# Performance work log

Hardware: AMD Instinct MI355X
Metric: run time of the kernel (lower is better)

Reference implementation:

```python
import jax, jax.numpy as jnp
import numpy as np

B, H_IMG, W_IMG = 8, 64, 64
C, HEADS, SR, MSG = 128, 4, 4, 4
N0 = H_IMG * W_IMG


def _linear(x, w, b):
    return x @ w.T + b


def _layernorm(x, g, b, eps=1e-5):
    mu = jnp.mean(x, -1, keepdims=True)
    var = jnp.mean(jnp.square(x - mu), -1, keepdims=True)
    return (x - mu) * jax.lax.rsqrt(var + eps) * g + b


def _conv2d(x, w, b, stride, pad, groups=1):
    y = jax.lax.conv_general_dilated(
        x, w, (stride, stride), [(pad, pad), (pad, pad)],
        dimension_numbers=("NCHW", "OIHW", "NCHW"), feature_group_count=groups)
    return y + b[None, :, None, None]


def setup_inputs():
    key = jax.random.key(0)
    ks = jax.random.split(key, 16)
    def nrm(k, shape, std=0.02):
        return jax.random.normal(k, shape, jnp.float32) * std
    z = lambda *s: jnp.zeros(s, jnp.float32)
    return {
        "x": jax.random.normal(ks[0], (B, N0, C), jnp.float32),
        "msg_tokens": jax.random.normal(ks[1], (B, MSG, C), jnp.float32),
        "Wq": nrm(ks[2], (C, C)), "bq": z(C),
        "sr1_w": nrm(ks[3], (C, C, 4, 4), float(np.sqrt(2.0 / (16 * C)))), "sr1_b": z(C),
        "ln1_g": jnp.ones((C,), jnp.float32), "ln1_b": z(C),
        "sr2_w": nrm(ks[4], (C, C, 2, 2), float(np.sqrt(2.0 / (4 * C)))), "sr2_b": z(C),
        "ln2_g": jnp.ones((C,), jnp.float32), "ln2_b": z(C),
        "kv1_w": nrm(ks[5], (C, C)), "kv1_b": z(C),
        "kv2_w": nrm(ks[6], (C, C)), "kv2_b": z(C),
        "lc1_w": nrm(ks[7], (C // 2, 1, 3, 3), float(np.sqrt(2.0 / 9.0))), "lc1_b": z(C // 2),
        "lc2_w": nrm(ks[8], (C // 2, 1, 3, 3), float(np.sqrt(2.0 / 9.0))), "lc2_b": z(C // 2),
        "proj_w": nrm(ks[9], (C, C)), "proj_b": z(C),
        "H": H_IMG, "W": W_IMG,
    }


def reference(x, msg_tokens, Wq, bq, sr1_w, sr1_b, ln1_g, ln1_b,
              sr2_w, sr2_b, ln2_g, ln2_b, kv1_w, kv1_b, kv2_w, kv2_b,
              lc1_w, lc1_b, lc2_w, lc2_b, proj_w, proj_b, H, W):
    Bsz, _, Cc = x.shape
    m = msg_tokens.shape[1]
    h = HEADS
    dh = Cc // h
    scale = dh ** -0.5
    x_q = jnp.concatenate([x, msg_tokens], axis=1)       # [B, N, C]
    N = x_q.shape[1]
    q = _linear(x_q, Wq, bq).reshape(Bsz, N, h, dh).transpose(0, 2, 1, 3)  # [B,h,N,dh]
    x_img = x.transpose(0, 2, 1).reshape(Bsz, Cc, H, W)

    def branch(sr_w, sr_b, ln_g, ln_b, kv_w, kv_b, lc_w, lc_b, q_half, stride):
        Hr, Wr = H // stride, W // stride
        L = Hr * Wr
        # spatial reduction conv -> tokens
        xr = _conv2d(x_img, sr_w, sr_b, stride, 0).reshape(Bsz, Cc, L).transpose(0, 2, 1)
        # message tokens pass through the SR conv via summed weights
        msg_r = jnp.einsum('bnc,oc->bno', msg_tokens, sr_w.sum((-1, -2))) + sr_b
        xk = jax.nn.gelu(_layernorm(jnp.concatenate([xr, msg_r], 1), ln_g, ln_b), approximate=False)
        kv = _linear(xk, kv_w, kv_b).reshape(Bsz, L + m, 2, h // 2, dh).transpose(2, 0, 3, 1, 4)
        k, v = kv[0], kv[1]                               # [B, h/2, L+m, dh]
        attn = jax.nn.softmax(jnp.einsum('bhnd,bhld->bhnl', q_half, k) * scale, axis=-1)
        # fused depthwise conv on the spatial part of V (message tokens bypass)
        v_flat = v.transpose(0, 2, 1, 3).reshape(Bsz, L + m, Cc // 2).transpose(0, 2, 1)  # [B,C/2,L+m]
        lc = _conv2d(v_flat[:, :, :L].reshape(Bsz, Cc // 2, Hr, Wr), lc_w, lc_b, 1, 1,
                     groups=Cc // 2).reshape(Bsz, Cc // 2, L)
        v_add = jnp.concatenate([lc, v_flat[:, :, L:]], axis=2)
        v = v + v_add.reshape(Bsz, h // 2, dh, L + m).transpose(0, 1, 3, 2)
        return jnp.einsum('bhnl,bhld->bhnd', attn, v).transpose(0, 2, 1, 3).reshape(Bsz, N, Cc // 2)

    x1 = branch(sr1_w, sr1_b, ln1_g, ln1_b, kv1_w, kv1_b, lc1_w, lc1_b, q[:, :h // 2], SR)
    x2 = branch(sr2_w, sr2_b, ln2_g, ln2_b, kv2_w, kv2_b, lc2_w, lc2_b, q[:, h // 2:], SR // 2)
    out = _linear(jnp.concatenate([x1, x2], -1), proj_w, proj_b)
    out = x_q + out                                       # identity = x_q, drop_path = Identity
    return out[:, :-m], out[:, -m:]
```

## Files before the change

kernel.cpp:

```cpp
#include <hip/hip_runtime.h>
#include <math.h>

#define BB 8
#define CC 128
#define N0 4096
#define MSGN 4
#define NTOT 4100
#define IMG 64
#define NPAD 4112
#define QTILES 257
#define LMP1 320
#define LMP2 1088

#define OFF_WFQ    0
#define OFF_WFKV1  8192
#define OFF_WFKV2  16384
#define OFF_WFPROJ 24576
#define OFF_WFSR1  32768
#define OFF_WFSR2  163840
#define OFF_QH     196608
#define OFF_XK1    2301952
#define OFF_XK2    2435072
#define OFF_KV1O   2961408
#define OFF_KV2O   3227648
#define OFF_KH1    4280320
#define OFF_VT1    4362240
#define OFF_KH2    4444160
#define OFF_VT2    4722688
#define OFF_XP0    5001216
#define OFF_XP1    7102464
#define OFF_L0     2301952
#define OFF_L1     2433280

typedef _Float16 half8v __attribute__((ext_vector_type(8)));
typedef _Float16 half4v __attribute__((ext_vector_type(4)));
typedef float f32x4 __attribute__((ext_vector_type(4)));

__device__ __forceinline__ size_t af_idx(int m, int k, int Kc) {
    return ((size_t)((m >> 4) * Kc + (k >> 5)) * 64 + ((k >> 3) & 3) * 16 + (m & 15)) * 8 + (k & 7);
}

__global__ void prep_weights(const float* __restrict__ Wq, const float* __restrict__ kv1,
                             const float* __restrict__ kv2, const float* __restrict__ proj,
                             const float* __restrict__ sr1w, const float* __restrict__ sr2w,
                             float* __restrict__ ws, _Float16* __restrict__ Qh) {
    int u = blockIdx.x * blockDim.x + threadIdx.x;
    if (u >= 49152) {
        int idx = u - 49152;
        if (idx >= BB * 4 * (NPAD - NTOT) * 32) return;
        int d = idx & 31;
        int rest = idx >> 5;
        int n = NTOT + rest % (NPAD - NTOT);
        int rest2 = rest / (NPAD - NTOT);
        int hg = rest2 & 3;
        int b = rest2 >> 2;
        Qh[((size_t)(b * 4 + hg) * NPAD + n) * 32 + d] = (_Float16)0.f;
        return;
    }
    int seg, base;
    const float* w = nullptr;
    _Float16* dst;
    if (u < 2048)        { seg = 0; base = u;          w = Wq;   dst = (_Float16*)(ws + OFF_WFQ); }
    else if (u < 4096)   { seg = 0; base = u - 2048;   w = kv1;  dst = (_Float16*)(ws + OFF_WFKV1); }
    else if (u < 6144)   { seg = 0; base = u - 4096;   w = kv2;  dst = (_Float16*)(ws + OFF_WFKV2); }
    else if (u < 8192)   { seg = 0; base = u - 6144;   w = proj; dst = (_Float16*)(ws + OFF_WFPROJ); }
    else if (u < 40960)  { seg = 1; base = u - 8192;   w = sr1w; dst = (_Float16*)(ws + OFF_WFSR1); }
    else                 { seg = 2; base = u - 40960;  w = sr2w; dst = (_Float16*)(ws + OFF_WFSR2); }
    int lane = base & 63;
    int t = (base >> 6) & 7;
    int kc = base >> 9;
    int n = t * 16 + (lane & 15);
    int k0 = kc * 32 + (lane >> 4) * 8;
    half8v val;
    #pragma unroll
    for (int j = 0; j < 8; ++j) {
        int k = k0 + j;
        float v;
        if (seg == 0) v = w[n * 128 + k];
        else if (seg == 1) v = w[(n * 128 + (k & 127)) * 16 + (k >> 7)];
        else v = w[(n * 128 + (k & 127)) * 4 + (k >> 7)];
        val[j] = (_Float16)v;
    }
    *(half8v*)(dst + (size_t)base * 8) = val;
}

template<int S, int WR, int LL, int LM, int KW>
__device__ __forceinline__ void sr_partial(
    int mtile, int kcbase, int lane, const float* __restrict__ x,
    const float* __restrict__ msg, const _Float16* __restrict__ Wf, f32x4 acc[8]) {
    int m15 = lane & 15, quadk = lane >> 4;
    int m = mtile * 16 + m15;
    bool valid = m < BB * LM;
    const float* base = x;
    bool isimg = false;
    if (valid) {
        int b = m / LM, tok = m - b * LM;
        if (tok < LL) {
            int hr = tok / WR, wr = tok - hr * WR;
            base = x + ((size_t)b * N0 + hr * S * IMG + wr * S) * 128;
            isimg = true;
        } else {
            base = msg + ((size_t)b * MSGN + (tok - LL)) * 128;
        }
    }
    const half8v* Bp = (const half8v*)Wf + lane;
    for (int kk = 0; kk < KW; ++kk) {
        int kc = kcbase + kk;
        int k0 = (kc * 4 + quadk) * 8;
        int c = k0 & 127, ij = k0 >> 7;
        half8v a;
        if (valid) {
            int off;
            if (isimg) {
                int ki = ij / S, kj = ij - ki * S;
                off = (ki * IMG + kj) * 128 + c;
            } else off = c;
            const float4* p4 = (const float4*)(base + off);
            float4 f0 = p4[0], f1 = p4[1];
            a[0] = (_Float16)f0.x; a[1] = (_Float16)f0.y; a[2] = (_Float16)f0.z; a[3] = (_Float16)f0.w;
            a[4] = (_Float16)f1.x; a[5] = (_Float16)f1.y; a[6] = (_Float16)f1.z; a[7] = (_Float16)f1.w;
        } else {
            #pragma unroll
            for (int j = 0; j < 8; ++j) a[j] = (_Float16)0.f;
        }
        #pragma unroll
        for (int t = 0; t < 8; ++t)
            acc[t] = __builtin_amdgcn_mfma_f32_16x16x32_f16(a, Bp[(size_t)(kc * 8 + t) * 64], acc[t], 0, 0, 0);
    }
}

__global__ __launch_bounds__(256) void input_gemms(
    const float* __restrict__ x, const float* __restrict__ msg,
    const _Float16* __restrict__ Wf1, const _Float16* __restrict__ Wf2,
    const float* __restrict__ b1, const float* __restrict__ g1, const float* __restrict__ be1,
    const float* __restrict__ b2, const float* __restrict__ g2, const float* __restrict__ be2,
    _Float16* __restrict__ XK1, _Float16* __restrict__ XK2,
    const _Float16* __restrict__ WfQ, const float* __restrict__ bq,
    _Float16* __restrict__ Qh) {
    __shared__ float red[4][2048];
    int tid = threadIdx.x;
    int lane = tid & 63, wave = tid >> 6;
    int bid = blockIdx.x;

    if (bid >= 646) {
        int mt = (bid - 646) * 4 + wave;
        int m15 = lane & 15, quadk = lane >> 4;
        int m = mt * 16 + m15;
        bool valid = m < BB * NTOT;
        const float* rowp = x;
        if (valid) {
            int b = m / NTOT, n = m - b * NTOT;
            rowp = (n < N0) ? (x + ((size_t)b * N0 + n) * 128)
                            : (msg + ((size_t)b * MSGN + (n - N0)) * 128);
        }
        const half8v* Bp = (const half8v*)WfQ + lane;
        f32x4 acc[8];
        #pragma unroll
        for (int t = 0; t < 8; ++t) acc[t] = (f32x4){0.f, 0.f, 0.f, 0.f};
        #pragma unroll
        for (int kc = 0; kc < 4; ++kc) {
            half8v a;
            if (valid) {
                const float4* p4 = (const float4*)(rowp + (kc * 4 + quadk) * 8);
                float4 f0 = p4[0], f1 = p4[1];
                a[0] = (_Float16)f0.x; a[1] = (_Float16)f0.y; a[2] = (_Float16)f0.z; a[3] = (_Float16)f0.w;
                a[4] = (_Float16)f1.x; a[5] = (_Float16)f1.y; a[6] = (_Float16)f1.z; a[7] = (_Float16)f1.w;
            } else {
                #pragma unroll
                for (int j = 0; j < 8; ++j) a[j] = (_Float16)0.f;
            }
            #pragma unroll
            for (int t = 0; t < 8; ++t)
                acc[t] = __builtin_amdgcn_mfma_f32_16x16x32_f16(a, Bp[(size_t)(kc * 8 + t) * 64], acc[t], 0, 0, 0);
        }
        int quad = lane >> 4, n15 = lane & 15;
        const float qscale = 0.17677669529663687f;
        #pragma unroll
        for (int r = 0; r < 4; ++r) {
            int mm = mt * 16 + quad * 4 + r;
            if (mm >= BB * NTOT) continue;
            int b = mm / NTOT, tok = mm - b * NTOT;
            #pragma unroll
            for (int t = 0; t < 8; ++t) {
                int n = t * 16 + n15;
                Qh[((size_t)(b * 4 + (n >> 5)) * NPAD + tok) * 32 + (n & 31)] =
                    (_Float16)((acc[t][r] + bq[n]) * qscale);
            }
        }
        return;
    }

    f32x4 acc[8];
    #pragma unroll
    for (int t = 0; t < 8; ++t) acc[t] = (f32x4){0.f, 0.f, 0.f, 0.f};
    const float* bias;
    const float* lng;
    const float* lnb;
    _Float16* outp;
    int mtile, Mv;
    if (bid < 132) {
        mtile = bid; Mv = 2080;
        sr_partial<4, 16, 256, 260, 16>(mtile, wave * 16, lane, x, msg, Wf1, acc);
        bias = b1; lng = g1; lnb = be1; outp = XK1;
    } else {
        mtile = bid - 132; Mv = 8224;
        sr_partial<2, 32, 1024, 1028, 4>(mtile, wave * 4, lane, x, msg, Wf2, acc);
        bias = b2; lng = g2; lnb = be2; outp = XK2;
    }
    int quad = lane >> 4, n15 = lane & 15;
    #pragma unroll
    for (int t = 0; t < 8; ++t)
        #pragma unroll
        for (int r = 0; r < 4; ++r)
            red[wave][(quad * 4 + r) * 128 + t * 16 + n15] = acc[t][r];
    __syncthreads();
    for (int e = tid; e < 2048; e += 256)
        red[0][e] = red[0][e] + red[1][e] + red[2][e] + red[3][e];
    __syncthreads();
    int r16 = tid >> 4, l16 = tid & 15;
    int m = mtile * 16 + r16;
    float v[8];
    float s = 0.f;
    #pragma unroll
    for (int j = 0; j < 8; ++j) { v[j] = red[0][r16 * 128 + j * 16 + l16] + bias[j * 16 + l16]; s += v[j]; }
    #pragma unroll
    for (int off = 1; off < 16; off <<= 1) s += __shfl_xor(s, off);
    float mu = s * (1.f / 128.f);
    float q = 0.f;
    #pragma unroll
    for (int j = 0; j < 8; ++j) { v[j] -= mu; q += v[j] * v[j]; }
    #pragma unroll
    for (int off = 1; off < 16; off <<= 1) q += __shfl_xor(q, off);
    float rs = rsqrtf(q * (1.f / 128.f) + 1e-5f);
    if (m < Mv) {
        #pragma unroll
        for (int j = 0; j < 8; ++j) {
            int n = j * 16 + l16;
            float y = v[j] * rs * lng[n] + lnb[n];
            y = 0.5f * y * (1.f + erff(y * 0.70710678118654752f));
            outp[af_idx(m, n, 4)] = (_Float16)y;
        }
    }
}

__global__ __launch_bounds__(256) void kv_gemm(
    const _Float16* __restrict__ XK1, const _Float16* __restrict__ XK2,
    const _Float16* __restrict__ Wf1, const _Float16* __restrict__ Wf2,
    const float* __restrict__ b1, const float* __restrict__ b2,
    float* __restrict__ o1, float* __restrict__ o2) {
    int lane = threadIdx.x & 63, wave = threadIdx.x >> 6;
    int t = blockIdx.x * 4 + wave;
    int lt;
    const half8v* Ap;
    const half8v* Bp;
    const float* bias;
    float* outp;
    if (t < 130) { lt = t;       Ap = (const half8v*)XK1 + (size_t)lt * 4 * 64 + lane; Bp = (const half8v*)Wf1 + lane; bias = b1; outp = o1; }
    else         { lt = t - 130; Ap = (const half8v*)XK2 + (size_t)lt * 4 * 64 + lane; Bp = (const half8v*)Wf2 + lane; bias = b2; outp = o2; }
    f32x4 acc[8];
    #pragma unroll
    for (int tt = 0; tt < 8; ++tt) acc[tt] = (f32x4){0.f, 0.f, 0.f, 0.f};
    #pragma unroll
    for (int kc = 0; kc < 4; ++kc) {
        half8v a = Ap[(size_t)kc * 64];
        #pragma unroll
        for (int tt = 0; tt < 8; ++tt)
            acc[tt] = __builtin_amdgcn_mfma_f32_16x16x32_f16(a, Bp[(size_t)(kc * 8 + tt) * 64], acc[tt], 0, 0, 0);
    }
    int quad = lane >> 4, n15 = lane & 15;
    #pragma unroll
    for (int r = 0; r < 4; ++r) {
        int m = lt * 16 + quad * 4 + r;
        #pragma unroll
        for (int tt = 0; tt < 8; ++tt)
            outp[(size_t)m * 128 + tt * 16 + n15] = acc[tt][r] + bias[tt * 16 + n15];
    }
}

__global__ void pack_kv(const float* __restrict__ kv1o, const float* __restrict__ kv2o,
                        const float* __restrict__ lc1w, const float* __restrict__ lc1b,
                        const float* __restrict__ lc2w, const float* __restrict__ lc2b,
                        _Float16* __restrict__ Kh1, _Float16* __restrict__ Vt1,
                        _Float16* __restrict__ Kh2, _Float16* __restrict__ Vt2) {
    int idx = blockIdx.x * 256 + threadIdx.x;
    const int T1 = BB * LMP1 * 64;
    const float* kv;
    const float* lcw;
    const float* lcb;
    _Float16* Kh;
    _Float16* Vt;
    int Wr, L, Lm, Lmp, li;
    if (idx < T1) { li = idx;      kv = kv1o; lcw = lc1w; lcb = lc1b; Kh = Kh1; Vt = Vt1; Wr = 16; L = 256;  Lm = 260;  Lmp = LMP1; }
    else          { li = idx - T1; kv = kv2o; lcw = lc2w; lcb = lc2b; Kh = Kh2; Vt = Vt2; Wr = 32; L = 1024; Lm = 1028; Lmp = LMP2; }
    int ch = li & 63;
    int rest = li >> 6;
    int n = rest % Lmp;
    int b = rest / Lmp;
    int h2 = ch >> 5, d = ch & 31;
    int Hr = L / Wr;
    float kval = 0.f, vnew = 0.f;
    if (n < Lm) {
        const float* kvb = kv + (size_t)b * Lm * 128;
        kval = kvb[(size_t)n * 128 + ch];
        float v = kvb[(size_t)n * 128 + 64 + ch];
        float add;
        if (n < L) {
            int hr = n / Wr, wr = n - hr * Wr;
            float sum = lcb[ch];
            #pragma unroll
            for (int ki = 0; ki < 3; ++ki)
                #pragma unroll
                for (int kj = 0; kj < 3; ++kj) {
                    int y = hr + ki - 1, xx = wr + kj - 1;
                    if ((unsigned)y < (unsigned)Hr && (unsigned)xx < (unsigned)Wr)
                        sum += lcw[ch * 9 + ki * 3 + kj] * kvb[((size_t)y * Wr + xx) * 128 + 64 + ch];
                }
            add = sum;
        } else {
            add = v;
        }
        vnew = v + add;
    }
    Kh[((size_t)(b * 2 + h2) * Lmp + n) * 32 + d] = (_Float16)kval;
    Vt[(size_t)(b * 2 + h2) * Lmp * 32 + (size_t)(n >> 2) * 128 + d * 4 + (n & 3)] = (_Float16)vnew;
}

__global__ __launch_bounds__(256) void attn_mfma(
    const _Float16* __restrict__ Qh,
    const _Float16* __restrict__ Kh1, const _Float16* __restrict__ Vt1,
    const _Float16* __restrict__ Kh2, const _Float16* __restrict__ Vt2,
    _Float16* __restrict__ XP0, _Float16* __restrict__ XP1,
    float* __restrict__ L0, float* __restrict__ L1) {
    int tid = threadIdx.x;
    int lane = tid & 63, wave = tid >> 6;
    int b = blockIdx.y;
    int z = blockIdx.z;
    int h2 = z & 1, h = z >> 1;
    int tile = blockIdx.x * 4 + wave;
    if (tile >= QTILES) return;
    int n0 = tile * 16;
    int q16 = lane & 15, quad = lane >> 4;
    const f32x4 zf = {0.f, 0.f, 0.f, 0.f};
    _Float16* xp = h ? XP1 : XP0;
    float* Lp = h ? L1 : L0;

    for (int br = 0; br < 2; ++br) {
        int Lmp = br ? LMP2 : LMP1;
        int k_lo = h ? (br ? 576 : 192) : 0;
        int k_hi = br ? (h ? 1088 : 576) : (h ? 320 : 192);
        const _Float16* kb = (br ? Kh2 : Kh1) + (size_t)(b * 2 + h2) * Lmp * 32;
        const _Float16* vb = (br ? Vt2 : Vt1) + (size_t)(b * 2 + h2) * Lmp * 32;
        int hg = br * 2 + h2;
        half8v qf = *(const half8v*)(Qh + ((size_t)(b * 4 + hg) * NPAD + n0 + q16) * 32 + quad * 8);
        f32x4 O0 = {0.f, 0.f, 0.f, 0.f}, O1 = {0.f, 0.f, 0.f, 0.f};
        float l_part = 0.f;

        for (int k0 = k_lo; k0 < k_hi; k0 += 64) {
            f32x4 s4[4];
            #pragma unroll
            for (int i = 0; i < 4; ++i) {
                half8v kf = *(const half8v*)(kb + (size_t)(k0 + i * 16 + q16) * 32 + quad * 8);
                s4[i] = __builtin_amdgcn_mfma_f32_16x16x32_f16(kf, qf, zf, 0, 0, 0);
            }
            half4v pf[4];
            float ps = 0.f;
            #pragma unroll
            for (int i = 0; i < 4; ++i)
                #pragma unroll
                for (int r = 0; r < 4; ++r) {
                    float p = __expf(s4[i][r]);
                    ps += p;
                    pf[i][r] = (_Float16)p;
                }
            l_part += ps;
            #pragma unroll
            for (int i = 0; i < 4; ++i) {
                const _Float16* vbase = vb + (size_t)(((k0 + i * 16) >> 2) + quad) * 128 + q16 * 4;
                half4v v0 = *(const half4v*)(vbase);
                half4v v1 = *(const half4v*)(vbase + 64);
                O0 = __builtin_amdgcn_mfma_f32_16x16x16f16(pf[i], v0, O0, 0, 0, 0);
                O1 = __builtin_amdgcn_mfma_f32_16x16x16f16(pf[i], v1, O1, 0, 0, 0);
            }
        }

        float l = l_part;
        l += __shfl_xor(l, 16);
        l += __shfl_xor(l, 32);
        if (h) l -= 60.0f;
        if (quad == 0) {
            int n = n0 + q16;
            if (n < NTOT) Lp[(size_t)(b * NTOT + n) * 4 + hg] = l;
        }
        int kbase = br * 64 + h2 * 32;
        #pragma unroll
        for (int r = 0; r < 4; ++r) {
            int n = n0 + quad * 4 + r;
            if (n < NTOT) {
                int m = b * NTOT + n;
                xp[af_idx(m, kbase + q16, 4)] = (_Float16)O0[r];
                xp[af_idx(m, kbase + 16 + q16, 4)] = (_Float16)O1[r];
            }
        }
    }
}

__global__ __launch_bounds__(256) void proj_gemm(
    const _Float16* __restrict__ XP0, const _Float16* __restrict__ XP1,
    const float* __restrict__ L0, const float* __restrict__ L1,
    const _Float16* __restrict__ Wf, const float* __restrict__ bias,
    float* __restrict__ out_f32, const float* __restrict__ x, const float* __restrict__ msg) {
    int lane = threadIdx.x & 63, wave = threadIdx.x >> 6;
    int mt = blockIdx.x * 4 + wave;
    const half8v* Ap0 = (const half8v*)XP0 + (size_t)mt * 4 * 64 + lane;
    const half8v* Ap1 = (const half8v*)XP1 + (size_t)mt * 4 * 64 + lane;
    const half8v* Bp = (const half8v*)Wf + lane;
    int m15 = lane & 15;
    int mrow = mt * 16 + m15;
    bool lvalid = mrow < BB * NTOT;
    f32x4 acc[8];
    #pragma unroll
    for (int t = 0; t < 8; ++t) acc[t] = (f32x4){0.f, 0.f, 0.f, 0.f};
    #pragma unroll
    for (int kc = 0; kc < 4; ++kc) {
        half8v a0 = Ap0[(size_t)kc * 64];
        half8v a1 = Ap1[(size_t)kc * 64];
        float inv = 0.f;
        if (lvalid) {
            float l0 = L0[(size_t)mrow * 4 + kc];
            float l1 = L1[(size_t)mrow * 4 + kc];
            inv = 1.f / (l0 + l1);
        }
        half8v a;
        #pragma unroll
        for (int j = 0; j < 8; ++j)
            a[j] = (_Float16)(((float)a0[j] + (float)a1[j]) * inv);
        #pragma unroll
        for (int t = 0; t < 8; ++t)
            acc[t] = __builtin_amdgcn_mfma_f32_16x16x32_f16(a, Bp[(size_t)(kc * 8 + t) * 64], acc[t], 0, 0, 0);
    }
    int quad = lane >> 4, n15 = lane & 15;
    #pragma unroll
    for (int r = 0; r < 4; ++r) {
        int m = mt * 16 + quad * 4 + r;
        if (m >= BB * NTOT) continue;
        int b = m / NTOT, tok = m - b * NTOT;
        const float* rp;
        float* dst;
        if (tok < N0) {
            rp = x + ((size_t)b * N0 + tok) * 128;
            dst = out_f32 + ((size_t)b * N0 + tok) * 128;
        } else {
            rp = msg + ((size_t)b * MSGN + (tok - N0)) * 128;
            dst = out_f32 + (size_t)BB * N0 * 128 + ((size_t)b * MSGN + (tok - N0)) * 128;
        }
        #pragma unroll
        for (int t = 0; t < 8; ++t) {
            int n = t * 16 + n15;
            dst[n] = acc[t][r] + bias[n] + rp[n];
        }
    }
}

extern "C" void kernel_launch(void* const* d_in, const int* in_sizes, int n_in,
                              void* d_out, int out_size, void* d_ws, size_t ws_size,
                              hipStream_t stream) {
    const float* x     = (const float*)d_in[0];
    const float* msg   = (const float*)d_in[1];
    const float* Wq    = (const float*)d_in[2];
    const float* bq    = (const float*)d_in[3];
    const float* sr1w  = (const float*)d_in[4];
    const float* sr1b  = (const float*)d_in[5];
    const float* ln1g  = (const float*)d_in[6];
    const float* ln1b  = (const float*)d_in[7];
    const float* sr2w  = (const float*)d_in[8];
    const float* sr2b  = (const float*)d_in[9];
    const float* ln2g  = (const float*)d_in[10];
    const float* ln2b  = (const float*)d_in[11];
    const float* kv1w  = (const float*)d_in[12];
    const float* kv1b  = (const float*)d_in[13];
    const float* kv2w  = (const float*)d_in[14];
    const float* kv2b  = (const float*)d_in[15];
    const float* lc1w  = (const float*)d_in[16];
    const float* lc1b  = (const float*)d_in[17];
    const float* lc2w  = (const float*)d_in[18];
    const float* lc2b  = (const float*)d_in[19];
    const float* projw = (const float*)d_in[20];
    const float* projb = (const float*)d_in[21];
    float* ws  = (float*)d_ws;
    float* out = (float*)d_out;

    _Float16* WfQ    = (_Float16*)(ws + OFF_WFQ);
    _Float16* WfKV1  = (_Float16*)(ws + OFF_WFKV1);
    _Float16* WfKV2  = (_Float16*)(ws + OFF_WFKV2);
    _Float16* WfPROJ = (_Float16*)(ws + OFF_WFPROJ);
    _Float16* WfSR1  = (_Float16*)(ws + OFF_WFSR1);
    _Float16* WfSR2  = (_Float16*)(ws + OFF_WFSR2);
    _Float16* Qh     = (_Float16*)(ws + OFF_QH);
    _Float16* XP0    = (_Float16*)(ws + OFF_XP0);
    _Float16* XP1    = (_Float16*)(ws + OFF_XP1);
    float* L0        = ws + OFF_L0;
    float* L1        = ws + OFF_L1;
    _Float16* XK1    = (_Float16*)(ws + OFF_XK1);
    _Float16* XK2    = (_Float16*)(ws + OFF_XK2);
    float* kv1o      = ws + OFF_KV1O;
    float* kv2o      = ws + OFF_KV2O;
    _Float16* Kh1    = (_Float16*)(ws + OFF_KH1);
    _Float16* Vt1    = (_Float16*)(ws + OFF_VT1);
    _Float16* Kh2    = (_Float16*)(ws + OFF_KH2);
    _Float16* Vt2    = (_Float16*)(ws + OFF_VT2);

    prep_weights<<<240, 256, 0, stream>>>(Wq, kv1w, kv2w, projw, sr1w, sr2w, ws, Qh);
    input_gemms<<<1159, 256, 0, stream>>>(x, msg, WfSR1, WfSR2,
                                          sr1b, ln1g, ln1b, sr2b, ln2g, ln2b,
                                          XK1, XK2, WfQ, bq, Qh);
    kv_gemm<<<161, 256, 0, stream>>>(XK1, XK2, WfKV1, WfKV2, kv1b, kv2b, kv1o, kv2o);
    pack_kv<<<2816, 256, 0, stream>>>(kv1o, kv2o, lc1w, lc1b, lc2w, lc2b,
                                      Kh1, Vt1, Kh2, Vt2);
    attn_mfma<<<dim3(65, 8, 4), 256, 0, stream>>>(Qh, Kh1, Vt1, Kh2, Vt2,
                                                  XP0, XP1, L0, L1);
    proj_gemm<<<513, 256, 0, stream>>>(XP0, XP1, L0, L1, WfPROJ, projb, out, x, msg);
}
```

Before: 212.6 us.

## Process four query tiles per wave in attention to reuse K/V loads

Each wave now handles four 16-row query tiles instead of one, loading each K and V fragment once and feeding it to four MFMA chains. The grid shrinks from 65 to 17 blocks in x. This cuts redundant global K/V traffic per query row. In exchange it raises register pressure (16 accumulators plus four Q fragments) and leaves fewer waves in flight, which may hurt latency hiding. The last group clamps its tile index and does redundant compute on the final tile.

```diff
diff --git a/kernel.cpp b/kernel.cpp
--- a/kernel.cpp
+++ b/kernel.cpp
@@ -336,9 +336,8 @@
     int b = blockIdx.y;
     int z = blockIdx.z;
     int h2 = z & 1, h = z >> 1;
-    int tile = blockIdx.x * 4 + wave;
-    if (tile >= QTILES) return;
-    int n0 = tile * 16;
+    int g = blockIdx.x * 4 + wave;
+    if (g >= 65) return;
     int q16 = lane & 15, quad = lane >> 4;
     const f32x4 zf = {0.f, 0.f, 0.f, 0.f};
     _Float16* xp = h ? XP1 : XP0;
@@ -351,54 +350,74 @@
         const _Float16* kb = (br ? Kh2 : Kh1) + (size_t)(b * 2 + h2) * Lmp * 32;
         const _Float16* vb = (br ? Vt2 : Vt1) + (size_t)(b * 2 + h2) * Lmp * 32;
         int hg = br * 2 + h2;
-        half8v qf = *(const half8v*)(Qh + ((size_t)(b * 4 + hg) * NPAD + n0 + q16) * 32 + quad * 8);
-        f32x4 O0 = {0.f, 0.f, 0.f, 0.f}, O1 = {0.f, 0.f, 0.f, 0.f};
-        float l_part = 0.f;
+
+        half8v qf[4];
+        #pragma unroll
+        for (int tt = 0; tt < 4; ++tt) {
+            int tl = g * 4 + tt;
+            if (tl > 256) tl = 256;
+            qf[tt] = *(const half8v*)(Qh + ((size_t)(b * 4 + hg) * NPAD + tl * 16 + q16) * 32 + quad * 8);
+        }
+        f32x4 O0[4], O1[4];
+        float lp[4];
+        #pragma unroll
+        for (int tt = 0; tt < 4; ++tt) {
+            O0[tt] = zf; O1[tt] = zf; lp[tt] = 0.f;
+        }
 
         for (int k0 = k_lo; k0 < k_hi; k0 += 64) {
-            f32x4 s4[4];
+            half8v kf[4];
+            #pragma unroll
+            for (int i = 0; i < 4; ++i)
+                kf[i] = *(const half8v*)(kb + (size_t)(k0 + i * 16 + q16) * 32 + quad * 8);
             #pragma unroll
             for (int i = 0; i < 4; ++i) {
-                half8v kf = *(const half8v*)(kb + (size_t)(k0 + i * 16 + q16) * 32 + quad * 8);
-                s4[i] = __builtin_amdgcn_mfma_f32_16x16x32_f16(kf, qf, zf, 0, 0, 0);
-            }
-            half4v pf[4];
-            float ps = 0.f;
-            #pragma unroll
-            for (int i = 0; i < 4; ++i)
+                half4v pfi[4];
                 #pragma unroll
-                for (int r = 0; r < 4; ++r) {
-                    float p = __expf(s4[i][r]);
-                    ps += p;
-                    pf[i][r] = (_Float16)p;
+                for (int tt = 0; tt < 4; ++tt) {
+                    f32x4 s4 = __builtin_amdgcn_mfma_f32_16x16x32_f16(kf[i], qf[tt], zf, 0, 0, 0);
+                    float ps = 0.f;
+                    #pragma unroll
+                    for (int r = 0; r < 4; ++r) {
+                        float p = __expf(s4[r]);
+                        ps += p;
+                        pfi[tt][r] = (_Float16)p;
+                    }
+                    lp[tt] += ps;
                 }
-            l_part += ps;
-            #pragma unroll
-            for (int i = 0; i < 4; ++i) {
                 const _Float16* vbase = vb + (size_t)(((k0 + i * 16) >> 2) + quad) * 128 + q16 * 4;
                 half4v v0 = *(const half4v*)(vbase);
                 half4v v1 = *(const half4v*)(vbase + 64);
-                O0 = __builtin_amdgcn_mfma_f32_16x16x16f16(pf[i], v0, O0, 0, 0, 0);
-                O1 = __builtin_amdgcn_mfma_f32_16x16x16f16(pf[i], v1, O1, 0, 0, 0);
+                #pragma unroll
+                for (int tt = 0; tt < 4; ++tt) {
+                    O0[tt] = __builtin_amdgcn_mfma_f32_16x16x16f16(pfi[tt], v0, O0[tt], 0, 0, 0);
+                    O1[tt] = __builtin_amdgcn_mfma_f32_16x16x16f16(pfi[tt], v1, O1[tt], 0, 0, 0);
+                }
             }
         }
 
-        float l = l_part;
-        l += __shfl_xor(l, 16);
-        l += __shfl_xor(l, 32);
-        if (h) l -= 60.0f;
-        if (quad == 0) {
-            int n = n0 + q16;
-            if (n < NTOT) Lp[(size_t)(b * NTOT + n) * 4 + hg] = l;
-        }
         int kbase = br * 64 + h2 * 32;
         #pragma unroll
-        for (int r = 0; r < 4; ++r) {
-            int n = n0 + quad * 4 + r;
-            if (n < NTOT) {
-                int m = b * NTOT + n;
-                xp[af_idx(m, kbase + q16, 4)] = (_Float16)O0[r];
-                xp[af_idx(m, kbase + 16 + q16, 4)] = (_Float16)O1[r];
+        for (int tt = 0; tt < 4; ++tt) {
+            int tl = g * 4 + tt;
+            if (tl > 256) break;
+            int n0 = tl * 16;
+            float l = lp[tt];
+            l += __shfl_xor(l, 16);
+            l += __shfl_xor(l, 32);
+            if (h) l -= 60.0f;
+            if (quad == 0) {
+                int n = n0 + q16;
+                if (n < NTOT) Lp[(size_t)(b * NTOT + n) * 4 + hg] = l;
+            }
+            #pragma unroll
+            for (int r = 0; r < 4; ++r) {
+                int n = n0 + quad * 4 + r;
+                if (n < NTOT) {
+                    int m = b * NTOT + n;
+                    xp[af_idx(m, kbase + q16, 4)] = (_Float16)O0[tt][r];
+                    xp[af_idx(m, kbase + 16 + q16, 4)] = (_Float16)O1[tt][r];
+                }
             }
         }
     }
@@ -516,7 +535,7 @@
     kv_gemm<<<161, 256, 0, stream>>>(XK1, XK2, WfKV1, WfKV2, kv1b, kv2b, kv1o, kv2o);
     pack_kv<<<2816, 256, 0, stream>>>(kv1o, kv2o, lc1w, lc1b, lc2w, lc2b,
                                       Kh1, Vt1, Kh2, Vt2);
-    attn_mfma<<<dim3(65, 8, 4), 256, 0, stream>>>(Qh, Kh1, Vt1, Kh2, Vt2,
+    attn_mfma<<<dim3(17, 8, 4), 256, 0, stream>>>(Qh, Kh1, Vt1, Kh2, Vt2,
                                                   XP0, XP1, L0, L1);
     proj_gemm<<<513, 256, 0, stream>>>(XP0, XP1, L0, L1, WfPROJ, projb, out, x, msg);
 }
```

After: 214.2 us. Within noise of the previous version (+0.7%).
